# Performance work log

Measured on AMD Instinct MI355X. Metric: run time of the kernel, lower is better.

Reference implementation:

```python
import jax, jax.numpy as jnp
import numpy as np

B, S, D, K, NS = 4, 2048, 768, 8192, 2
TAU = 1.0


def setup_inputs() -> dict:
    key = jax.random.key(0)
    k1, k2, k3, k4 = jax.random.split(key, 4)
    x = jax.random.normal(k1, (B, S, D), dtype=jnp.float32)
    w_codebook = jax.random.normal(k2, (K, D), dtype=jnp.float32) * (1.0 / np.sqrt(D))
    embeddings = jax.random.normal(k3, (K, D), dtype=jnp.float32)
    # standard Gumbel(0,1) noise, one draw per (token, sample, code)
    gumbel_noise = jax.random.gumbel(k4, (B, S, NS, K), dtype=jnp.float32)
    return {"x": x, "w_codebook": w_codebook, "embeddings": embeddings,
            "gumbel_noise": gumbel_noise, "num_samples": NS}


def reference(x, w_codebook, embeddings, gumbel_noise, num_samples):
    # logits = Linear(x) without bias: [B, S, K]
    logits = jnp.einsum('bsd,kd->bsk', x, w_codebook)
    # expand over num_samples and add Gumbel noise (F.gumbel_softmax, training)
    g = (logits[:, :, None, :] + gumbel_noise) / TAU          # [B, S, NS, K]
    y_soft = jax.nn.softmax(g, axis=-1)
    # hard one-hot with straight-through estimator (hard=True, hard_p=1.0)
    idx = jnp.argmax(y_soft, axis=-1)                          # [B, S, NS]
    y_hard = jax.nn.one_hot(idx, K, dtype=y_soft.dtype)
    indices = y_hard + y_soft - jax.lax.stop_gradient(y_soft)  # [B, S, NS, K]
    # one-hot matmul == gather of codebook rows
    emb = jnp.einsum('bsnk,kd->bsnd', indices, embeddings)     # [B, S, NS, D]
    return emb, indices
```

## Files before the change

kernel.cpp:

```cpp
#include <hip/hip_runtime.h>
#include <stdint.h>

#define Bc 4
#define Sc 2048
#define Dc 768
#define Kc 8192
#define NSc 2
#define Mc (Bc*Sc)
#define EMB_ELEMS ((size_t)Mc*NSc*Dc)

typedef __attribute__((ext_vector_type(8))) __bf16 bf16x8;
typedef __attribute__((ext_vector_type(4))) float f32x4;
typedef __attribute__((ext_vector_type(4))) unsigned short u16x4;

__device__ __forceinline__ unsigned short f2bf(float f){
  unsigned int u = __float_as_uint(f);
  u += 0x7FFFu + ((u >> 16) & 1u);
  return (unsigned short)(u >> 16);
}
__device__ __forceinline__ float bf2f(unsigned short h){
  return __uint_as_float(((unsigned int)h) << 16);
}

__global__ __launch_bounds__(256) void k_convert(const float4* __restrict__ x,
                                                 const float4* __restrict__ w,
                                                 u16x4* __restrict__ xb,
                                                 u16x4* __restrict__ wb){
  int i = blockIdx.x * 256 + threadIdx.x;
  float4 v = x[i];
  u16x4 o;
  o.x = f2bf(v.x); o.y = f2bf(v.y); o.z = f2bf(v.z); o.w = f2bf(v.w);
  xb[i] = o;
  v = w[i];
  o.x = f2bf(v.x); o.y = f2bf(v.y); o.z = f2bf(v.z); o.w = f2bf(v.w);
  wb[i] = o;
}

#define BM 128
#define BN 128
#define BK 32

__global__ __launch_bounds__(256) void k_gemm(const unsigned short* __restrict__ xb,
                                              const unsigned short* __restrict__ wb,
                                              unsigned short* __restrict__ logits){
  __shared__ unsigned short As[BM*BK];
  __shared__ unsigned short Bs[BN*BK];

  const int tid  = threadIdx.x;
  const int lane = tid & 63;
  const int wid  = tid >> 6;
  const int wm   = wid >> 1;
  const int wn   = wid & 1;
  const int bm0  = blockIdx.y * BM;
  const int bn0  = blockIdx.x * BN;

  f32x4 acc[4][4] = {};

  const int srow  = tid >> 2;
  const int scole = (tid & 3) * 8;
  const unsigned short* aS0 = xb + (size_t)(bm0 + srow) * Dc + scole;
  const unsigned short* aS1 = xb + (size_t)(bm0 + 64 + srow) * Dc + scole;
  const unsigned short* bS0 = wb + (size_t)(bn0 + srow) * Dc + scole;
  const unsigned short* bS1 = wb + (size_t)(bn0 + 64 + srow) * Dc + scole;
  unsigned short* aD0 = &As[wid * 512];
  unsigned short* aD1 = &As[2048 + wid * 512];
  unsigned short* bD0 = &Bs[wid * 512];
  unsigned short* bD1 = &Bs[2048 + wid * 512];

  const int fr = lane & 15;
  const int fk = (lane >> 4) * 8;

  for (int kt = 0; kt < Dc; kt += BK) {
    __syncthreads();
    __builtin_amdgcn_global_load_lds((const __attribute__((address_space(1))) void*)(aS0 + kt),
                                     (__attribute__((address_space(3))) void*)aD0, 16, 0, 0);
    __builtin_amdgcn_global_load_lds((const __attribute__((address_space(1))) void*)(aS1 + kt),
                                     (__attribute__((address_space(3))) void*)aD1, 16, 0, 0);
    __builtin_amdgcn_global_load_lds((const __attribute__((address_space(1))) void*)(bS0 + kt),
                                     (__attribute__((address_space(3))) void*)bD0, 16, 0, 0);
    __builtin_amdgcn_global_load_lds((const __attribute__((address_space(1))) void*)(bS1 + kt),
                                     (__attribute__((address_space(3))) void*)bD1, 16, 0, 0);
    __syncthreads();

    bf16x8 a[4], b[4];
    #pragma unroll
    for (int i = 0; i < 4; i++) {
      a[i] = *(const bf16x8*)&As[(wm*64 + i*16 + fr) * BK + fk];
      b[i] = *(const bf16x8*)&Bs[(wn*64 + i*16 + fr) * BK + fk];
    }
    #pragma unroll
    for (int i = 0; i < 4; i++)
      #pragma unroll
      for (int j = 0; j < 4; j++)
        acc[i][j] = __builtin_amdgcn_mfma_f32_16x16x32_bf16(a[i], b[j], acc[i][j], 0, 0, 0);
  }

  const int crow0 = bm0 + wm*64 + (lane >> 4) * 4;
  const int ccol0 = bn0 + wn*64 + (lane & 15);
  #pragma unroll
  for (int i = 0; i < 4; i++)
    #pragma unroll
    for (int j = 0; j < 4; j++)
      #pragma unroll
      for (int r = 0; r < 4; r++)
        logits[(size_t)(crow0 + i*16 + r) * 32768 + (ccol0 + j*16)] = f2bf(acc[i][j][r]);
}

#define MARGIN 0.125f

__global__ __launch_bounds__(256) void k_select(const unsigned short* logits,
                                                const float* __restrict__ gumbel,
                                                const float* __restrict__ x,
                                                const float* __restrict__ w,
                                                const float* __restrict__ emb_tab,
                                                float* __restrict__ out_emb,
                                                float* out_ind){
  const int t   = blockIdx.x;
  const int tid = threadIdx.x;
  const int lane = tid & 63, wid = tid >> 6;

  __shared__ unsigned short Lrow[Kc];
  __shared__ float wmax[4];
  __shared__ int   cand_k[16];
  __shared__ float cand_g[16];
  __shared__ int   cand_cnt;
  __shared__ int   sel_idx;

  {
    const u16x4* src = (const u16x4*)(logits + (size_t)t * 32768);
    u16x4* dst = (u16x4*)Lrow;
    #pragma unroll
    for (int j = 0; j < 8; j++) dst[j*256 + tid] = src[j*256 + tid];
  }
  __syncthreads();

  for (int s = 0; s < NSc; ++s) {
    const float* grow = gumbel + ((size_t)t * NSc + s) * Kc;
    float4 vals[8];
    float m = -1e30f;
    #pragma unroll
    for (int j = 0; j < 8; j++) {
      float4 g4 = ((const float4*)grow)[j*256 + tid];
      u16x4 l4 = *(const u16x4*)&Lrow[j*1024 + tid*4];
      float4 v;
      v.x = bf2f(l4.x) + g4.x;
      v.y = bf2f(l4.y) + g4.y;
      v.z = bf2f(l4.z) + g4.z;
      v.w = bf2f(l4.w) + g4.w;
      vals[j] = v;
      m = fmaxf(m, fmaxf(fmaxf(v.x, v.y), fmaxf(v.z, v.w)));
    }
    #pragma unroll
    for (int off = 32; off; off >>= 1) m = fmaxf(m, __shfl_xor(m, off));
    if (lane == 0) wmax[wid] = m;
    __syncthreads();
    const float gmax = fmaxf(fmaxf(wmax[0], wmax[1]), fmaxf(wmax[2], wmax[3]));
    if (tid == 0) cand_cnt = 0;
    __syncthreads();

    const float thr = gmax - MARGIN;
    #pragma unroll
    for (int j = 0; j < 8; j++) {
      const int k0 = j*1024 + tid*4;
      float vv[4] = {vals[j].x, vals[j].y, vals[j].z, vals[j].w};
      #pragma unroll
      for (int q = 0; q < 4; q++) {
        if (vv[q] >= thr) {
          int p = atomicAdd(&cand_cnt, 1);
          if (p < 16) cand_k[p] = k0 + q;
        }
      }
    }
    __syncthreads();

    const int cnt = min(cand_cnt, 16);
    int idx;
    if (cnt == 1) {
      idx = cand_k[0];
    } else {
      for (int c = wid; c < cnt; c += 4) {
        const int kc = cand_k[c];
        const float* wr = w + (size_t)kc * Dc;
        const float* xr = x + (size_t)t * Dc;
        double accd = 0.0;
        for (int d = lane; d < Dc; d += 64) accd += (double)xr[d] * (double)wr[d];
        #pragma unroll
        for (int off = 32; off; off >>= 1) accd += __shfl_xor(accd, off);
        if (lane == 0) cand_g[c] = (float)accd + grow[kc];
      }
      __syncthreads();
      if (tid == 0) {
        float bg = -1e30f; int bk_ = Kc;
        for (int c = 0; c < cnt; c++) {
          float g = cand_g[c]; int kk = cand_k[c];
          if (g > bg || (g == bg && kk < bk_)) { bg = g; bk_ = kk; }
        }
        sel_idx = bk_;
      }
      __syncthreads();
      idx = sel_idx;
    }

    float* irow = out_ind + ((size_t)t * NSc + s) * Kc;
    #pragma unroll
    for (int j = 0; j < 8; j++) {
      const int k0 = j*1024 + tid*4;
      float4 z = {0.f, 0.f, 0.f, 0.f};
      const int d = idx - k0;
      if (d == 0) z.x = 1.0f; else if (d == 1) z.y = 1.0f;
      else if (d == 2) z.z = 1.0f; else if (d == 3) z.w = 1.0f;
      ((float4*)irow)[j*256 + tid] = z;
    }
    const float* er = emb_tab + (size_t)idx * Dc;
    float* eo = out_emb + ((size_t)t * NSc + s) * Dc;
    for (int d = tid; d < Dc; d += 256) eo[d] = er[d];
    __syncthreads();
  }
}

extern "C" void kernel_launch(void* const* d_in, const int* in_sizes, int n_in,
                              void* d_out, int out_size, void* d_ws, size_t ws_size,
                              hipStream_t stream) {
  const float* x   = (const float*)d_in[0];
  const float* w   = (const float*)d_in[1];
  const float* emb = (const float*)d_in[2];
  const float* gum = (const float*)d_in[3];

  float* out_emb = (float*)d_out;
  float* out_ind = out_emb + EMB_ELEMS;
  unsigned short* logits = (unsigned short*)out_ind;

  unsigned short* xb = (unsigned short*)d_ws;
  unsigned short* wb = xb + (size_t)Mc * Dc;

  const int n4 = (Mc * Dc) / 4;
  k_convert<<<n4 / 256, 256, 0, stream>>>((const float4*)x, (const float4*)w,
                                          (u16x4*)xb, (u16x4*)wb);
  dim3 gg(Kc / BN, Mc / BM);
  k_gemm<<<gg, 256, 0, stream>>>(xb, wb, logits);
  k_select<<<Mc, 256, 0, stream>>>(logits, gum, x, w, emb, out_emb, out_ind);
}
```

Before: 401.7 us.

## Fuse Gumbel-add tile max into GEMM epilogue; select scans only candidate tiles

```diff
diff --git a/kernel.cpp b/kernel.cpp
--- a/kernel.cpp
+++ b/kernel.cpp
@@ -7,6 +7,7 @@
 #define Kc 8192
 #define NSc 2
 #define Mc (Bc*Sc)
+#define NTILES 64
 #define EMB_ELEMS ((size_t)Mc*NSc*Dc)
 
 typedef __attribute__((ext_vector_type(8))) __bf16 bf16x8;
@@ -42,9 +43,12 @@
 
 __global__ __launch_bounds__(256) void k_gemm(const unsigned short* __restrict__ xb,
                                               const unsigned short* __restrict__ wb,
-                                              unsigned short* __restrict__ logits){
+                                              const float* __restrict__ gumbel,
+                                              unsigned short* __restrict__ logits,
+                                              float* __restrict__ stats){
   __shared__ unsigned short As[BM*BK];
   __shared__ unsigned short Bs[BN*BK];
+  __shared__ float smax[NSc][BM][2];
 
   const int tid  = threadIdx.x;
   const int lane = tid & 63;
@@ -104,11 +108,39 @@
       #pragma unroll
       for (int r = 0; r < 4; r++)
         logits[(size_t)(crow0 + i*16 + r) * 32768 + (ccol0 + j*16)] = f2bf(acc[i][j][r]);
+
+  #pragma unroll
+  for (int s = 0; s < NSc; s++) {
+    #pragma unroll
+    for (int i = 0; i < 4; i++) {
+      #pragma unroll
+      for (int r = 0; r < 4; r++) {
+        const int trow = wm*64 + i*16 + (lane >> 4)*4 + r;
+        const float* g = gumbel + ((size_t)(bm0 + trow)*NSc + s)*Kc
+                                + bn0 + wn*64 + (lane & 15);
+        float m = -1e30f;
+        #pragma unroll
+        for (int j = 0; j < 4; j++)
+          m = fmaxf(m, acc[i][j][r] + g[j*16]);
+        #pragma unroll
+        for (int off = 1; off <= 8; off <<= 1)
+          m = fmaxf(m, __shfl_xor(m, off));
+        if ((lane & 15) == 0) smax[s][trow][wn] = m;
+      }
+    }
+  }
+  __syncthreads();
+  {
+    const int s = tid >> 7, trow = tid & 127;
+    const float m = fmaxf(smax[s][trow][0], smax[s][trow][1]);
+    stats[((size_t)(bm0 + trow)*NSc + s)*NTILES + blockIdx.x] = m;
+  }
 }
 
 #define MARGIN 0.125f
 
 __global__ __launch_bounds__(256) void k_select(const unsigned short* logits,
+                                                const float* __restrict__ stats,
                                                 const float* __restrict__ gumbel,
                                                 const float* __restrict__ x,
                                                 const float* __restrict__ w,
@@ -119,65 +151,46 @@
   const int tid = threadIdx.x;
   const int lane = tid & 63, wid = tid >> 6;
 
-  __shared__ unsigned short Lrow[Kc];
-  __shared__ float wmax[4];
   __shared__ int   cand_k[16];
   __shared__ float cand_g[16];
   __shared__ int   cand_cnt;
-  __shared__ int   sel_idx;
-
-  {
-    const u16x4* src = (const u16x4*)(logits + (size_t)t * 32768);
-    u16x4* dst = (u16x4*)Lrow;
-    #pragma unroll
-    for (int j = 0; j < 8; j++) dst[j*256 + tid] = src[j*256 + tid];
-  }
-  __syncthreads();
+  __shared__ int   sel_idx[NSc];
 
   for (int s = 0; s < NSc; ++s) {
-    const float* grow = gumbel + ((size_t)t * NSc + s) * Kc;
-    float4 vals[8];
-    float m = -1e30f;
-    #pragma unroll
-    for (int j = 0; j < 8; j++) {
-      float4 g4 = ((const float4*)grow)[j*256 + tid];
-      u16x4 l4 = *(const u16x4*)&Lrow[j*1024 + tid*4];
-      float4 v;
-      v.x = bf2f(l4.x) + g4.x;
-      v.y = bf2f(l4.y) + g4.y;
-      v.z = bf2f(l4.z) + g4.z;
-      v.w = bf2f(l4.w) + g4.w;
-      vals[j] = v;
-      m = fmaxf(m, fmaxf(fmaxf(v.x, v.y), fmaxf(v.z, v.w)));
-    }
-    #pragma unroll
-    for (int off = 32; off; off >>= 1) m = fmaxf(m, __shfl_xor(m, off));
-    if (lane == 0) wmax[wid] = m;
-    __syncthreads();
-    const float gmax = fmaxf(fmaxf(wmax[0], wmax[1]), fmaxf(wmax[2], wmax[3]));
     if (tid == 0) cand_cnt = 0;
     __syncthreads();
 
-    const float thr = gmax - MARGIN;
-    #pragma unroll
-    for (int j = 0; j < 8; j++) {
-      const int k0 = j*1024 + tid*4;
-      float vv[4] = {vals[j].x, vals[j].y, vals[j].z, vals[j].w};
-      #pragma unroll
-      for (int q = 0; q < 4; q++) {
-        if (vv[q] >= thr) {
-          int p = atomicAdd(&cand_cnt, 1);
-          if (p < 16) cand_k[p] = k0 + q;
+    if (wid == 0) {
+      const float myv = stats[((size_t)t*NSc + s)*NTILES + lane];
+      float g = myv;
+      #pragma unroll
+      for (int off = 32; off; off >>= 1) g = fmaxf(g, __shfl_xor(g, off));
+      const float thr = g - MARGIN;
+      unsigned long long mask = __ballot(myv >= thr);
+      const unsigned short* lrow = logits + (size_t)t * 32768;
+      const float* grow = gumbel + ((size_t)t*NSc + s)*Kc;
+      while (mask) {
+        const int tile = __ffsll(mask) - 1;
+        mask &= mask - 1;
+        const int k0 = tile * 128;
+        #pragma unroll
+        for (int q = 0; q < 2; ++q) {
+          const int k = k0 + q*64 + lane;
+          const float val = bf2f(lrow[k]) + grow[k];
+          if (val >= thr) {
+            const int p = atomicAdd(&cand_cnt, 1);
+            if (p < 16) cand_k[p] = k;
+          }
         }
       }
     }
     __syncthreads();
 
     const int cnt = min(cand_cnt, 16);
-    int idx;
     if (cnt == 1) {
-      idx = cand_k[0];
+      if (tid == 0) sel_idx[s] = cand_k[0];
     } else {
+      const float* grow = gumbel + ((size_t)t*NSc + s)*Kc;
       for (int c = wid; c < cnt; c += 4) {
         const int kc = cand_k[c];
         const float* wr = w + (size_t)kc * Dc;
@@ -190,20 +203,23 @@
       }
       __syncthreads();
       if (tid == 0) {
-        float bg = -1e30f; int bk_ = Kc;
-        for (int c = 0; c < cnt; c++) {
-          float g = cand_g[c]; int kk = cand_k[c];
-          if (g > bg || (g == bg && kk < bk_)) { bg = g; bk_ = kk; }
+        float bg = -1e30f; int bk = Kc;
+        for (int c = 0; c < cnt; ++c) {
+          const float gg = cand_g[c]; const int kk = cand_k[c];
+          if (gg > bg || (gg == bg && kk < bk)) { bg = gg; bk = kk; }
         }
-        sel_idx = bk_;
-      }
-      __syncthreads();
-      idx = sel_idx;
-    }
-
-    float* irow = out_ind + ((size_t)t * NSc + s) * Kc;
-    #pragma unroll
-    for (int j = 0; j < 8; j++) {
+        sel_idx[s] = bk;
+      }
+    }
+    __syncthreads();
+  }
+
+  #pragma unroll
+  for (int s = 0; s < NSc; ++s) {
+    const int idx = sel_idx[s];
+    float* irow = out_ind + ((size_t)t*NSc + s)*Kc;
+    #pragma unroll
+    for (int j = 0; j < 8; ++j) {
       const int k0 = j*1024 + tid*4;
       float4 z = {0.f, 0.f, 0.f, 0.f};
       const int d = idx - k0;
@@ -212,9 +228,8 @@
       ((float4*)irow)[j*256 + tid] = z;
     }
     const float* er = emb_tab + (size_t)idx * Dc;
-    float* eo = out_emb + ((size_t)t * NSc + s) * Dc;
+    float* eo = out_emb + ((size_t)t*NSc + s)*Dc;
     for (int d = tid; d < Dc; d += 256) eo[d] = er[d];
-    __syncthreads();
   }
 }
 
@@ -232,11 +247,12 @@
 
   unsigned short* xb = (unsigned short*)d_ws;
   unsigned short* wb = xb + (size_t)Mc * Dc;
+  float* stats = (float*)(wb + (size_t)Kc * Dc);
 
   const int n4 = (Mc * Dc) / 4;
   k_convert<<<n4 / 256, 256, 0, stream>>>((const float4*)x, (const float4*)w,
                                           (u16x4*)xb, (u16x4*)wb);
   dim3 gg(Kc / BN, Mc / BM);
-  k_gemm<<<gg, 256, 0, stream>>>(xb, wb, logits);
-  k_select<<<Mc, 256, 0, stream>>>(logits, gum, x, w, emb, out_emb, out_ind);
-}
+  k_gemm<<<gg, 256, 0, stream>>>(xb, wb, gum, logits, stats);
+  k_select<<<Mc, 256, 0, stream>>>(logits, stats, gum, x, w, emb, out_emb, out_ind);
+}
```

Measured after the change: 549.2 us. +36.7%, slower.

## Zero one-hot output inside GEMM and place bf16 logits stash in output tail

Applied to the files above, without the earlier changes.

```diff
diff --git a/kernel.cpp b/kernel.cpp
--- a/kernel.cpp
+++ b/kernel.cpp
@@ -42,7 +42,8 @@
 
 __global__ __launch_bounds__(256) void k_gemm(const unsigned short* __restrict__ xb,
                                               const unsigned short* __restrict__ wb,
-                                              unsigned short* __restrict__ logits){
+                                              unsigned short* __restrict__ stash,
+                                              float* __restrict__ out_ind){
   __shared__ unsigned short As[BM*BK];
   __shared__ unsigned short Bs[BN*BK];
 
@@ -51,8 +52,11 @@
   const int wid  = tid >> 6;
   const int wm   = wid >> 1;
   const int wn   = wid & 1;
-  const int bm0  = blockIdx.y * BM;
-  const int bn0  = blockIdx.x * BN;
+
+  const int bid  = (int)blockIdx.x;
+  const int swz  = (bid & 7) * 512 + (bid >> 3);
+  const int bm0  = (swz >> 6) * BM;
+  const int bn0  = (swz & 63) * BN;
 
   f32x4 acc[4][4] = {};
 
@@ -70,8 +74,9 @@
   const int fr = lane & 15;
   const int fk = (lane >> 4) * 8;
 
-  for (int kt = 0; kt < Dc; kt += BK) {
-    __syncthreads();
+  for (int it = 0; it < Dc/BK; ++it) {
+    __syncthreads();
+    const int kt = it * BK;
     __builtin_amdgcn_global_load_lds((const __attribute__((address_space(1))) void*)(aS0 + kt),
                                      (__attribute__((address_space(3))) void*)aD0, 16, 0, 0);
     __builtin_amdgcn_global_load_lds((const __attribute__((address_space(1))) void*)(aS1 + kt),
@@ -80,6 +85,15 @@
                                      (__attribute__((address_space(3))) void*)bD0, 16, 0, 0);
     __builtin_amdgcn_global_load_lds((const __attribute__((address_space(1))) void*)(bS1 + kt),
                                      (__attribute__((address_space(3))) void*)bD1, 16, 0, 0);
+
+    if (it < 16) {
+      const int n  = it*256 + tid;
+      const int tl = n >> 5, f4 = n & 31;
+      float4 z = {0.f, 0.f, 0.f, 0.f};
+      float4* zp = (float4*)out_ind + (size_t)(bm0 + tl)*4096 + (bn0 >> 2) + f4;
+      zp[0] = z;
+      if (bn0 < 4096) zp[2048] = z;
+    }
     __syncthreads();
 
     bf16x8 a[4], b[4];
@@ -103,12 +117,12 @@
     for (int j = 0; j < 4; j++)
       #pragma unroll
       for (int r = 0; r < 4; r++)
-        logits[(size_t)(crow0 + i*16 + r) * 32768 + (ccol0 + j*16)] = f2bf(acc[i][j][r]);
+        stash[(size_t)(crow0 + i*16 + r) * 32768 + (ccol0 + j*16)] = f2bf(acc[i][j][r]);
 }
 
 #define MARGIN 0.125f
 
-__global__ __launch_bounds__(256) void k_select(const unsigned short* logits,
+__global__ __launch_bounds__(256) void k_select(const unsigned short* stash,
                                                 const float* __restrict__ gumbel,
                                                 const float* __restrict__ x,
                                                 const float* __restrict__ w,
@@ -124,10 +138,10 @@
   __shared__ int   cand_k[16];
   __shared__ float cand_g[16];
   __shared__ int   cand_cnt;
-  __shared__ int   sel_idx;
+  __shared__ int   sel_idx[NSc];
 
   {
-    const u16x4* src = (const u16x4*)(logits + (size_t)t * 32768);
+    const u16x4* src = (const u16x4*)(stash + (size_t)t * 32768);
     u16x4* dst = (u16x4*)Lrow;
     #pragma unroll
     for (int j = 0; j < 8; j++) dst[j*256 + tid] = src[j*256 + tid];
@@ -174,9 +188,8 @@
     __syncthreads();
 
     const int cnt = min(cand_cnt, 16);
-    int idx;
     if (cnt == 1) {
-      idx = cand_k[0];
+      if (tid == 0) sel_idx[s] = cand_k[0];
     } else {
       for (int c = wid; c < cnt; c += 4) {
         const int kc = cand_k[c];
@@ -190,31 +203,36 @@
       }
       __syncthreads();
       if (tid == 0) {
-        float bg = -1e30f; int bk_ = Kc;
-        for (int c = 0; c < cnt; c++) {
-          float g = cand_g[c]; int kk = cand_k[c];
-          if (g > bg || (g == bg && kk < bk_)) { bg = g; bk_ = kk; }
+        float bg = -1e30f; int bk = Kc;
+        for (int c = 0; c < cnt; ++c) {
+          const float gg = cand_g[c]; const int kk = cand_k[c];
+          if (gg > bg || (gg == bg && kk < bk)) { bg = gg; bk = kk; }
         }
-        sel_idx = bk_;
+        sel_idx[s] = bk;
       }
-      __syncthreads();
-      idx = sel_idx;
-    }
-
-    float* irow = out_ind + ((size_t)t * NSc + s) * Kc;
-    #pragma unroll
-    for (int j = 0; j < 8; j++) {
-      const int k0 = j*1024 + tid*4;
-      float4 z = {0.f, 0.f, 0.f, 0.f};
-      const int d = idx - k0;
-      if (d == 0) z.x = 1.0f; else if (d == 1) z.y = 1.0f;
-      else if (d == 2) z.z = 1.0f; else if (d == 3) z.w = 1.0f;
-      ((float4*)irow)[j*256 + tid] = z;
-    }
+    }
+    __syncthreads();
+  }
+
+  {
+    float* row1hi = out_ind + (size_t)t*16384 + 8192 + 4096;
+    float4 z = {0.f, 0.f, 0.f, 0.f};
+    #pragma unroll
+    for (int q = 0; q < 4; ++q)
+      ((float4*)row1hi)[q*256 + tid] = z;
+  }
+  __syncthreads();
+  if (tid == 0) {
+    out_ind[(size_t)t*16384 +        sel_idx[0]] = 1.0f;
+    out_ind[(size_t)t*16384 + 8192 + sel_idx[1]] = 1.0f;
+  }
+
+  #pragma unroll
+  for (int s = 0; s < NSc; ++s) {
+    const int idx = sel_idx[s];
     const float* er = emb_tab + (size_t)idx * Dc;
-    float* eo = out_emb + ((size_t)t * NSc + s) * Dc;
+    float* eo = out_emb + ((size_t)t*NSc + s)*Dc;
     for (int d = tid; d < Dc; d += 256) eo[d] = er[d];
-    __syncthreads();
   }
 }
 
@@ -228,7 +246,7 @@
 
   float* out_emb = (float*)d_out;
   float* out_ind = out_emb + EMB_ELEMS;
-  unsigned short* logits = (unsigned short*)out_ind;
+  unsigned short* stash = (unsigned short*)out_ind + 24576;
 
   unsigned short* xb = (unsigned short*)d_ws;
   unsigned short* wb = xb + (size_t)Mc * Dc;
@@ -236,7 +254,6 @@
   const int n4 = (Mc * Dc) / 4;
   k_convert<<<n4 / 256, 256, 0, stream>>>((const float4*)x, (const float4*)w,
                                           (u16x4*)xb, (u16x4*)wb);
-  dim3 gg(Kc / BN, Mc / BM);
-  k_gemm<<<gg, 256, 0, stream>>>(xb, wb, logits);
-  k_select<<<Mc, 256, 0, stream>>>(logits, gum, x, w, emb, out_emb, out_ind);
-}
+  k_gemm<<<4096, 256, 0, stream>>>(xb, wb, stash, out_ind);
+  k_select<<<Mc, 256, 0, stream>>>(stash, gum, x, w, emb, out_emb, out_ind);
+}
```

Result: slower. 428.3 us (+6.6%).

## Rewrite logits GEMM with 256x256 tiles, double-buffered LDS and swizzled layout

Applied to the files above, without the earlier changes.

```diff
diff --git a/kernel.cpp b/kernel.cpp
--- a/kernel.cpp
+++ b/kernel.cpp
@@ -36,74 +36,130 @@
   wb[i] = o;
 }
 
-#define BM 128
-#define BN 128
-#define BK 32
-
-__global__ __launch_bounds__(256) void k_gemm(const unsigned short* __restrict__ xb,
-                                              const unsigned short* __restrict__ wb,
-                                              unsigned short* __restrict__ logits){
-  __shared__ unsigned short As[BM*BK];
-  __shared__ unsigned short Bs[BN*BK];
+__global__ __launch_bounds__(512, 2) void k_gemm(const unsigned short* __restrict__ xb,
+                                                 const unsigned short* __restrict__ wb,
+                                                 unsigned short* __restrict__ stash){
+  __shared__ __align__(16) unsigned char lds[131072];
 
   const int tid  = threadIdx.x;
   const int lane = tid & 63;
   const int wid  = tid >> 6;
-  const int wm   = wid >> 1;
-  const int wn   = wid & 1;
-  const int bm0  = blockIdx.y * BM;
-  const int bn0  = blockIdx.x * BN;
-
-  f32x4 acc[4][4] = {};
-
-  const int srow  = tid >> 2;
-  const int scole = (tid & 3) * 8;
-  const unsigned short* aS0 = xb + (size_t)(bm0 + srow) * Dc + scole;
-  const unsigned short* aS1 = xb + (size_t)(bm0 + 64 + srow) * Dc + scole;
-  const unsigned short* bS0 = wb + (size_t)(bn0 + srow) * Dc + scole;
-  const unsigned short* bS1 = wb + (size_t)(bn0 + 64 + srow) * Dc + scole;
-  unsigned short* aD0 = &As[wid * 512];
-  unsigned short* aD1 = &As[2048 + wid * 512];
-  unsigned short* bD0 = &Bs[wid * 512];
-  unsigned short* bD1 = &Bs[2048 + wid * 512];
-
-  const int fr = lane & 15;
-  const int fk = (lane >> 4) * 8;
-
-  for (int kt = 0; kt < Dc; kt += BK) {
-    __syncthreads();
-    __builtin_amdgcn_global_load_lds((const __attribute__((address_space(1))) void*)(aS0 + kt),
-                                     (__attribute__((address_space(3))) void*)aD0, 16, 0, 0);
-    __builtin_amdgcn_global_load_lds((const __attribute__((address_space(1))) void*)(aS1 + kt),
-                                     (__attribute__((address_space(3))) void*)aD1, 16, 0, 0);
-    __builtin_amdgcn_global_load_lds((const __attribute__((address_space(1))) void*)(bS0 + kt),
-                                     (__attribute__((address_space(3))) void*)bD0, 16, 0, 0);
-    __builtin_amdgcn_global_load_lds((const __attribute__((address_space(1))) void*)(bS1 + kt),
-                                     (__attribute__((address_space(3))) void*)bD1, 16, 0, 0);
-    __syncthreads();
-
-    bf16x8 a[4], b[4];
-    #pragma unroll
-    for (int i = 0; i < 4; i++) {
-      a[i] = *(const bf16x8*)&As[(wm*64 + i*16 + fr) * BK + fk];
-      b[i] = *(const bf16x8*)&Bs[(wn*64 + i*16 + fr) * BK + fk];
-    }
-    #pragma unroll
-    for (int i = 0; i < 4; i++)
-      #pragma unroll
-      for (int j = 0; j < 4; j++)
-        acc[i][j] = __builtin_amdgcn_mfma_f32_16x16x32_bf16(a[i], b[j], acc[i][j], 0, 0, 0);
-  }
-
-  const int crow0 = bm0 + wm*64 + (lane >> 4) * 4;
-  const int ccol0 = bn0 + wn*64 + (lane & 15);
-  #pragma unroll
-  for (int i = 0; i < 4; i++)
-    #pragma unroll
-    for (int j = 0; j < 4; j++)
-      #pragma unroll
-      for (int r = 0; r < 4; r++)
-        logits[(size_t)(crow0 + i*16 + r) * 32768 + (ccol0 + j*16)] = f2bf(acc[i][j][r]);
+  const int wr   = wid >> 2;
+  const int wc   = wid & 3;
+  const int fr   = lane & 15;
+  const int fq   = lane >> 4;
+
+  const int bid = (int)blockIdx.x;
+  const int swz = (bid & 7) * 128 + (bid >> 3);
+  const int bm0 = (swz >> 5) * 256;
+  const int bn0 = (swz & 31) * 256;
+
+  f32x4 acc[8][4] = {};
+
+  const int rin   = tid >> 3;
+  const int kblkp = (tid & 7) ^ (rin & 7);
+  const unsigned short* gsrc[8];
+  unsigned dstoff[8];
+  #pragma unroll
+  for (int s = 0; s < 8; ++s) {
+    const int isA = s >> 2;
+    const int q   = s & 3;
+    const int r64 = isA ? (((q & 1) << 1) | (q >> 1)) : q;
+    const int grow = (isA ? bm0 : bn0) + r64 * 64 + rin;
+    gsrc[s]   = (isA ? xb : wb) + (size_t)grow * Dc + kblkp * 8;
+    dstoff[s] = (isA ? 0u : 32768u) + (unsigned)r64 * 8192u + (unsigned)wid * 1024u;
+  }
+
+#define ISSUE(s_, bo_) __builtin_amdgcn_global_load_lds( \
+    (const __attribute__((address_space(1))) void*)gsrc[s_], \
+    (__attribute__((address_space(3))) void*)&lds[(bo_) + dstoff[s_]], 16, 0, 0)
+
+  #pragma unroll
+  for (int s = 0; s < 8; ++s) ISSUE(s, 0u);
+  #pragma unroll
+  for (int s = 0; s < 8; ++s) gsrc[s] += 64;
+
+  unsigned bufR = 0u, bufW = 65536u;
+  const unsigned aRow = (unsigned)(wr*128 + fr) * 128u;
+  const unsigned bRow = (unsigned)(wc*64  + fr) * 128u + 32768u;
+  const unsigned sl0  = (unsigned)((fq       ) ^ (fr & 7)) * 16u;
+  const unsigned sl1  = (unsigned)((fq + 4   ) ^ (fr & 7)) * 16u;
+
+  for (int t = 0; t < 12; ++t) {
+    const bool more = (t < 11);
+    bf16x8 a[4], b0[4], b1[4];
+
+    asm volatile("s_waitcnt vmcnt(2)" ::: "memory");
+    __builtin_amdgcn_s_barrier();
+    asm volatile("" ::: "memory");
+    if (more) { ISSUE(0, bufW); ISSUE(1, bufW); }
+    #pragma unroll
+    for (int n = 0; n < 4; ++n) b0[n] = *(const bf16x8*)&lds[bufR + bRow + (unsigned)n*2048u + sl0];
+    #pragma unroll
+    for (int m = 0; m < 4; ++m) a[m]  = *(const bf16x8*)&lds[bufR + aRow + (unsigned)m*2048u + sl0];
+    __builtin_amdgcn_s_setprio(1);
+    #pragma unroll
+    for (int m = 0; m < 4; ++m)
+      #pragma unroll
+      for (int n = 0; n < 4; ++n)
+        acc[m][n] = __builtin_amdgcn_mfma_f32_16x16x32_bf16(a[m], b0[n], acc[m][n], 0, 0, 0);
+    __builtin_amdgcn_s_setprio(0);
+
+    if (more) asm volatile("s_waitcnt vmcnt(2)" ::: "memory");
+    else      asm volatile("s_waitcnt vmcnt(0)" ::: "memory");
+    __builtin_amdgcn_s_barrier();
+    asm volatile("" ::: "memory");
+    if (more) { ISSUE(2, bufW); ISSUE(3, bufW); }
+    #pragma unroll
+    for (int m = 0; m < 4; ++m) a[m] = *(const bf16x8*)&lds[bufR + aRow + 8192u + (unsigned)m*2048u + sl0];
+    __builtin_amdgcn_s_setprio(1);
+    #pragma unroll
+    for (int m = 0; m < 4; ++m)
+      #pragma unroll
+      for (int n = 0; n < 4; ++n)
+        acc[4+m][n] = __builtin_amdgcn_mfma_f32_16x16x32_bf16(a[m], b0[n], acc[4+m][n], 0, 0, 0);
+    __builtin_amdgcn_s_setprio(0);
+
+    if (more) { ISSUE(4, bufW); ISSUE(5, bufW); }
+    #pragma unroll
+    for (int n = 0; n < 4; ++n) b1[n] = *(const bf16x8*)&lds[bufR + bRow + (unsigned)n*2048u + sl1];
+    #pragma unroll
+    for (int m = 0; m < 4; ++m) a[m]  = *(const bf16x8*)&lds[bufR + aRow + (unsigned)m*2048u + sl1];
+    __builtin_amdgcn_s_setprio(1);
+    #pragma unroll
+    for (int m = 0; m < 4; ++m)
+      #pragma unroll
+      for (int n = 0; n < 4; ++n)
+        acc[m][n] = __builtin_amdgcn_mfma_f32_16x16x32_bf16(a[m], b1[n], acc[m][n], 0, 0, 0);
+    __builtin_amdgcn_s_setprio(0);
+
+    if (more) { ISSUE(6, bufW); ISSUE(7, bufW); }
+    #pragma unroll
+    for (int m = 0; m < 4; ++m) a[m] = *(const bf16x8*)&lds[bufR + aRow + 8192u + (unsigned)m*2048u + sl1];
+    __builtin_amdgcn_s_setprio(1);
+    #pragma unroll
+    for (int m = 0; m < 4; ++m)
+      #pragma unroll
+      for (int n = 0; n < 4; ++n)
+        acc[4+m][n] = __builtin_amdgcn_mfma_f32_16x16x32_bf16(a[m], b1[n], acc[4+m][n], 0, 0, 0);
+    __builtin_amdgcn_s_setprio(0);
+
+    bufR ^= 65536u; bufW ^= 65536u;
+    if (t < 10) {
+      #pragma unroll
+      for (int s = 0; s < 8; ++s) gsrc[s] += 64;
+    }
+  }
+#undef ISSUE
+
+  #pragma unroll
+  for (int m = 0; m < 8; ++m)
+    #pragma unroll
+    for (int n = 0; n < 4; ++n)
+      #pragma unroll
+      for (int r = 0; r < 4; ++r)
+        stash[(size_t)(bm0 + wr*128 + m*16 + fq*4 + r) * 32768
+              + (bn0 + wc*64 + n*16 + fr)] = f2bf(acc[m][n][r]);
 }
 
 #define MARGIN 0.125f
@@ -124,7 +180,7 @@
   __shared__ int   cand_k[16];
   __shared__ float cand_g[16];
   __shared__ int   cand_cnt;
-  __shared__ int   sel_idx;
+  __shared__ int   sel_idx[NSc];
 
   {
     const u16x4* src = (const u16x4*)(logits + (size_t)t * 32768);
@@ -195,23 +251,25 @@
           float g = cand_g[c]; int kk = cand_k[c];
           if (g > bg || (g == bg && kk < bk_)) { bg = g; bk_ = kk; }
         }
-        sel_idx = bk_;
+        sel_idx[s] = bk_;
       }
       __syncthreads();
-      idx = sel_idx;
-    }
+      idx = sel_idx[s];
+    }
+    if (cnt == 1 && tid == 0) sel_idx[s] = idx;
+    __syncthreads();
 
     float* irow = out_ind + ((size_t)t * NSc + s) * Kc;
     #pragma unroll
     for (int j = 0; j < 8; j++) {
       const int k0 = j*1024 + tid*4;
       float4 z = {0.f, 0.f, 0.f, 0.f};
-      const int d = idx - k0;
+      const int d = sel_idx[s] - k0;
       if (d == 0) z.x = 1.0f; else if (d == 1) z.y = 1.0f;
       else if (d == 2) z.z = 1.0f; else if (d == 3) z.w = 1.0f;
       ((float4*)irow)[j*256 + tid] = z;
     }
-    const float* er = emb_tab + (size_t)idx * Dc;
+    const float* er = emb_tab + (size_t)sel_idx[s] * Dc;
     float* eo = out_emb + ((size_t)t * NSc + s) * Dc;
     for (int d = tid; d < Dc; d += 256) eo[d] = er[d];
     __syncthreads();
@@ -228,7 +286,7 @@
 
   float* out_emb = (float*)d_out;
   float* out_ind = out_emb + EMB_ELEMS;
-  unsigned short* logits = (unsigned short*)out_ind;
+  unsigned short* stash = (unsigned short*)out_ind;
 
   unsigned short* xb = (unsigned short*)d_ws;
   unsigned short* wb = xb + (size_t)Mc * Dc;
@@ -236,7 +294,6 @@
   const int n4 = (Mc * Dc) / 4;
   k_convert<<<n4 / 256, 256, 0, stream>>>((const float4*)x, (const float4*)w,
                                           (u16x4*)xb, (u16x4*)wb);
-  dim3 gg(Kc / BN, Mc / BM);
-  k_gemm<<<gg, 256, 0, stream>>>(xb, wb, logits);
-  k_select<<<Mc, 256, 0, stream>>>(logits, gum, x, w, emb, out_emb, out_ind);
-}
+  k_gemm<<<1024, 512, 0, stream>>>(xb, wb, stash);
+  k_select<<<Mc, 256, 0, stream>>>(stash, gum, x, w, emb, out_emb, out_ind);
+}
```

After: 381.9 us. 4.9% less time.
